# Performance work log

Measured on AMD Instinct MI355X. Metric: run time of the kernel, lower is better.

Reference implementation:

```python
import math
import jax, jax.numpy as jnp
import numpy as np

B, N, L, D, H = 1, 64, 512, 768, 12
DK = D // H


def setup_inputs() -> dict:
    rng = jax.random.key(0)
    ks = jax.random.split(rng, 8)
    s = 0.02  # weight init scale
    return {
        "query": jax.random.normal(ks[0], (B, N, L, D), jnp.float32),
        "key": jax.random.normal(ks[1], (B, N, L, D), jnp.float32),
        "value": jax.random.normal(ks[2], (B, N, L, D), jnp.float32),
        "Wq": jax.random.normal(ks[3], (D, D), jnp.float32) * s,
        "bq": jnp.zeros((D,), jnp.float32),
        "Wk": jax.random.normal(ks[4], (D, D), jnp.float32) * s,
        "bk": jnp.zeros((D,), jnp.float32),
        "Wv": jax.random.normal(ks[5], (D, D), jnp.float32) * s,
        "bv": jnp.zeros((D,), jnp.float32),
        "Wo": jax.random.normal(ks[6], (D, D), jnp.float32) * s,
        "bo": jnp.zeros((D,), jnp.float32),
    }


def reference(query, key, value, Wq, bq, Wk, bk, Wv, bv, Wo, bo):
    b, n, l, d = query.shape
    h, dk = H, DK
    # combined scaling: 1/sqrt(d_k) * 1/sqrt(N)
    scale = 1.0 / (math.sqrt(dk) * math.sqrt(n))
    # nn.Linear: y = x @ W.T + b  (W is [out, in])
    q = (jnp.einsum('bnld,ed->bnle', query, Wq) + bq).reshape(b, n, l, h, dk) * scale
    k = (jnp.einsum('bnld,ed->bnle', key, Wk) + bk).reshape(b, n, l, h, dk)
    v = (jnp.einsum('bnld,ed->bnle', value, Wv) + bv).reshape(b, n, l, h, dk)
    # tied attention: scores summed over the N (sequence-copy) axis BEFORE softmax
    att = jnp.einsum('bnihk,bnjhk->bhij', q, k)  # [B,H,L,L]
    att = jax.nn.softmax(att, axis=-1)  # dropout is identity in eval
    # single attention map broadcast across all N value tensors
    out = jnp.einsum('bhij,bnjhk->bnihk', att, v).reshape(b, n, l, d)
    return jnp.einsum('bnld,ed->bnle', out, Wo) + bo
```

## Files before the change

kernel.cpp:

```cpp
#include <hip/hip_runtime.h>


typedef __bf16 bf16x8 __attribute__((ext_vector_type(8)));
typedef float f32x4 __attribute__((ext_vector_type(4)));

__device__ __forceinline__ unsigned short f2bf(float f) {
  unsigned u = __float_as_uint(f);
  u += 0x7fffu + ((u >> 16) & 1u);
  return (unsigned short)(u >> 16);
}

__device__ __forceinline__ void gll16(const void* g, void* l) {
  __builtin_amdgcn_global_load_lds(
      (const __attribute__((address_space(1))) unsigned int*)g,
      (__attribute__((address_space(3))) unsigned int*)l, 16, 0, 0);
}

#define BAR __builtin_amdgcn_s_barrier()

enum { MODE_QCAT = 0, MODE_VT = 1, MODE_ATT = 2, MODE_OUTWS = 3, MODE_OUT_BIAS = 4 };

template <int MODE>
__global__ __launch_bounds__(512, 2) void gemm256(
    const void* __restrict__ Av, const void* __restrict__ Bv,
    const float* __restrict__ b0, const float* __restrict__ b1,
    void* __restrict__ Cv, int K, int lda, int ldb,
    long long a_bs, long long b_bs, float alpha0, float alpha1,
    long long c_bs, int ntn) {
  __shared__ unsigned short L[2][2][16384];

  const int tid = threadIdx.x;
  const int wave = tid >> 6;
  const int lane = tid & 63;
  const int wm = wave >> 2;
  const int wn = wave & 3;
  const int l15 = lane & 15;
  const int kq8 = lane >> 4;
  const int sw = l15 & 7;

  const int bid = blockIdx.x;
  const int xcd = bid & 7;
  const int kk_ = bid >> 3;
  const int tn = kk_ % ntn;
  const int tm = (kk_ / ntn) * 8 + xcd;
  const int batch = blockIdx.z;

  const long long m0 = (long long)tm * 256;
  const long long n0 = (long long)tn * 256;

  const unsigned short* Ab = (const unsigned short*)Av + (long long)batch * a_bs;
  const unsigned short* Bb = (const unsigned short*)Bv + (long long)batch * b_bs;

  const long long rowAw = m0 + wave * 8 + (lane >> 3);
  const long long rowBw = n0 + wave * 8 + (lane >> 3);
  const int csw = ((lane & 7) ^ (lane >> 3)) << 3;

  f32x4 acc[8][4] = {};

  auto stA = [&](int buf, int q, int k0) {
    gll16(Ab + (rowAw + (q << 6)) * (long long)lda + k0 + csw,
          &L[buf][0][(q << 12) + (wave << 9)]);
  };
  auto stB = [&](int buf, int q, int k0) {
    gll16(Bb + (rowBw + (q << 6)) * (long long)ldb + k0 + csw,
          &L[buf][1][(q << 12) + (wave << 9)]);
  };

  float bpre[4] = {};
  float aa = 1.0f;
  if constexpr (MODE == MODE_QCAT || MODE == MODE_VT || MODE == MODE_OUT_BIAS) {
    const float* bb = batch ? b1 : b0;
    aa = batch ? alpha1 : alpha0;
#pragma unroll
    for (int u = 0; u < 4; ++u) bpre[u] = bb[n0 + wn * 64 + u * 16 + l15];
  }

  const int NT = K >> 6;
#pragma unroll
  for (int q = 0; q < 4; ++q) stB(0, q, 0);
#pragma unroll
  for (int q = 0; q < 4; ++q) stA(0, q, 0);
  if (NT > 1) {
    stA(1, 0, 64);
    stA(1, 2, 64);
    asm volatile("s_waitcnt vmcnt(2)" ::: "memory");
  } else {
    asm volatile("s_waitcnt vmcnt(0)" ::: "memory");
  }
  BAR;

  for (int T = 0; T < NT; ++T) {
    const int cur = T & 1, nxt = cur ^ 1;
    const int k1 = (T + 1) << 6, k2 = (T + 2) << 6;
#pragma unroll
    for (int p = 0; p < 4; ++p) {
      const int kc = p >> 1, mh = p & 1;
      bf16x8 af[4], bfr[4];
#pragma unroll
      for (int mf = 0; mf < 4; ++mf) {
        const int row = wm * 128 + mh * 64 + mf * 16 + l15;
        af[mf] = *(const bf16x8*)&L[cur][0][row * 64 + (((kc << 2) + kq8) ^ sw) * 8];
      }
#pragma unroll
      for (int u = 0; u < 4; ++u) {
        const int row = wn * 64 + u * 16 + l15;
        bfr[u] = *(const bf16x8*)&L[cur][1][row * 64 + (((kc << 2) + kq8) ^ sw) * 8];
      }
      if (p == 0 && T + 1 < NT) { stB(nxt, 0, k1); stB(nxt, 1, k1); }
      if (p == 1 && T + 1 < NT) { stB(nxt, 2, k1); stB(nxt, 3, k1); }
      if (p == 2 && T + 1 < NT) { stA(nxt, 1, k1); stA(nxt, 3, k1); }
      if (p == 3 && T + 2 < NT) { stA(cur, 0, k2); stA(cur, 2, k2); }
      __builtin_amdgcn_s_setprio(1);
#pragma unroll
      for (int mf = 0; mf < 4; ++mf)
#pragma unroll
        for (int u = 0; u < 4; ++u)
          acc[mh * 4 + mf][u] = __builtin_amdgcn_mfma_f32_16x16x32_bf16(
              af[mf], bfr[u], acc[mh * 4 + mf][u], 0, 0, 0);
      __builtin_amdgcn_s_setprio(0);
      if (p == 3) {
        if (T + 1 < NT) {
          if (T + 2 < NT) asm volatile("s_waitcnt vmcnt(2)" ::: "memory");
          else            asm volatile("s_waitcnt vmcnt(0)" ::: "memory");
          BAR;
        }
      } else {
        BAR;
      }
    }
  }

#pragma unroll
  for (int mf = 0; mf < 8; ++mf) {
#pragma unroll
    for (int u = 0; u < 4; ++u) {
      const long long col = n0 + wn * 64 + u * 16 + l15;
#pragma unroll
      for (int r = 0; r < 4; ++r) {
        const long long row = m0 + wm * 128 + mf * 16 + (lane >> 4) * 4 + r;
        float v = acc[mf][u][r];
        if constexpr (MODE == MODE_QCAT) {
          const float vv = (v + bpre[u]) * aa;
          const long long h = col >> 6, kq = col & 63, n = row >> 9, i = row & 511;
          ((unsigned short*)Cv + batch * c_bs)[((h * 512 + i) << 12) + (n << 6) + kq] =
              f2bf(vv);
        } else if constexpr (MODE == MODE_VT) {
          const float vv = v + bpre[u];
          const long long h = col >> 6, kq = col & 63, n = row >> 9, j = row & 511;
          ((unsigned short*)Cv)[(((h << 12) + (n << 6) + kq) << 9) + j] = f2bf(vv);
        } else {
          ((float*)Cv)[row * 768 + col] = v + bpre[u];
        }
      }
    }
  }
}

constexpr int BM = 128, BN = 128, BK = 32;

template <int MODE, bool SWZ, int KS>
__global__ __launch_bounds__(256, 2) void gemm_bt(
    const void* __restrict__ Av, const void* __restrict__ Bv,
    const float* __restrict__ bias, void* __restrict__ Cv,
    int K, int lda, int ldb, long long a_bs, long long b_bs,
    float alpha, int ntn, long long c_bs) {
  constexpr int LP = 32;

  __shared__ unsigned short As0[BM * LP];
  __shared__ unsigned short Bs0[BN * LP];
  __shared__ unsigned short As1[BM * LP];
  __shared__ unsigned short Bs1[BN * LP];

  const int tid = threadIdx.x;
  const int wave = tid >> 6;
  const int lane = tid & 63;
  const int wm = wave >> 1, wn = wave & 1;

  int tm, tn, batch = 0, ks = 0;
  if constexpr (SWZ && MODE == MODE_ATT) {
    const int bid = blockIdx.x;
    const int xcd = bid & 7, j = bid >> 3;
    const int z = (j >> 4) * 8 + xcd;
    const int tile = j & 15;
    tn = tile & 3;
    tm = tile >> 2;
    ks = z % KS;
    batch = z / KS;
  } else if constexpr (SWZ && MODE == MODE_OUTWS) {
    const int bid = blockIdx.x;
    const int xcd = bid & 7, j = bid >> 3;
    const int g = (j >> 6) * 8 + xcd;
    const int idx = j & 63;
    batch = g >> 1;
    tm = idx >> 4;
    tn = (g & 1) * 16 + (idx & 15);
  } else {
    if constexpr (SWZ) {
      const int bid = blockIdx.x;
      const int xcd = bid & 7;
      const int k = bid >> 3;
      tn = k % ntn;
      tm = (k / ntn) * 8 + xcd;
    } else {
      tn = blockIdx.x;
      tm = blockIdx.y;
    }
    batch = blockIdx.z;
    if constexpr (KS > 1) { ks = batch % KS; batch /= KS; }
  }

  const long long m0 = (long long)tm * BM;
  const long long n0 = (long long)tn * BN;

  const unsigned short* Ab = (const unsigned short*)Av + (long long)batch * a_bs + (long long)ks * K;
  const unsigned short* Bb = (const unsigned short*)Bv + (long long)batch * b_bs + (long long)ks * K;

  f32x4 acc[4][4] = {};

  const int l15 = lane & 15;
  const int kq = (lane >> 4) * 8;
  const int r_in = lane >> 2;
  const int c8 = (lane & 3) * 8;

  auto stage = [&](unsigned short* Asb, unsigned short* Bsb, int k0) {
#pragma unroll
    for (int t = 0; t < 2; ++t) {
      const int rb = t * 64 + wave * 16;
      gll16(Ab + (m0 + rb + r_in) * (long long)lda + k0 + c8, &Asb[rb * LP]);
      gll16(Bb + (n0 + rb + r_in) * (long long)ldb + k0 + c8, &Bsb[rb * LP]);
    }
  };
  auto compute = [&](const unsigned short* Asb, const unsigned short* Bsb) {
    bf16x8 af[4], bfr[4];
#pragma unroll
    for (int t = 0; t < 4; ++t)
      af[t] = *(const bf16x8*)&Asb[(wm * 64 + t * 16 + l15) * LP + kq];
#pragma unroll
    for (int u = 0; u < 4; ++u)
      bfr[u] = *(const bf16x8*)&Bsb[(wn * 64 + u * 16 + l15) * LP + kq];
#pragma unroll
    for (int t = 0; t < 4; ++t)
#pragma unroll
      for (int u = 0; u < 4; ++u)
        acc[t][u] = __builtin_amdgcn_mfma_f32_16x16x32_bf16(af[t], bfr[u], acc[t][u], 0, 0, 0);
  };

  stage(As0, Bs0, 0);
  asm volatile("s_waitcnt vmcnt(0)" ::: "memory");
  BAR;

  const int NT = K >> 5;
  for (int t = 0; t < NT; t += 2) {
    stage(As1, Bs1, (t + 1) << 5);
    asm volatile("s_waitcnt vmcnt(4)" ::: "memory");
    BAR;
    compute(As0, Bs0);
    BAR;
    if (t + 2 < NT) {
      stage(As0, Bs0, (t + 2) << 5);
      asm volatile("s_waitcnt vmcnt(4)" ::: "memory");
    } else {
      asm volatile("s_waitcnt vmcnt(0)" ::: "memory");
    }
    BAR;
    compute(As1, Bs1);
    BAR;
  }

#pragma unroll
  for (int t = 0; t < 4; ++t) {
#pragma unroll
    for (int u = 0; u < 4; ++u) {
      const long long col = n0 + wn * 64 + u * 16 + l15;
#pragma unroll
      for (int r = 0; r < 4; ++r) {
        const long long row = m0 + wm * 64 + t * 16 + (lane >> 4) * 4 + r;
        float v = acc[t][u][r];
        if constexpr (MODE == MODE_ATT) {
          float* p = &((float*)Cv)[((long long)batch << 18) + (row << 9) + col];
          if constexpr (KS > 1) atomicAdd(p, v); else *p = v;
        } else if constexpr (MODE == MODE_OUTWS) {
          const long long n = col >> 6, kk = col & 63;
          ((unsigned short*)Cv)[(n * 512 + row) * 768 + (long long)batch * 64 + kk] = f2bf(v);
        } else {
          ((float*)Cv)[row * 768 + col] = v + alpha;
        }
      }
    }
  }
}

__global__ __launch_bounds__(256) void softmax_rows(const float* __restrict__ att,
                                                    unsigned short* __restrict__ outb) {
  const long long rowbase = (long long)blockIdx.x << 9;
  const int tid = threadIdx.x;
  float a = att[rowbase + tid];
  float b = att[rowbase + tid + 256];

  float m = fmaxf(a, b);
#pragma unroll
  for (int off = 32; off; off >>= 1) m = fmaxf(m, __shfl_down(m, off));
  __shared__ float redm[4];
  if ((tid & 63) == 0) redm[tid >> 6] = m;
  __syncthreads();
  m = fmaxf(fmaxf(redm[0], redm[1]), fmaxf(redm[2], redm[3]));

  const float e0 = __expf(a - m), e1 = __expf(b - m);
  float s = e0 + e1;
#pragma unroll
  for (int off = 32; off; off >>= 1) s += __shfl_down(s, off);
  __shared__ float reds[4];
  if ((tid & 63) == 0) reds[tid >> 6] = s;
  __syncthreads();
  s = reds[0] + reds[1] + reds[2] + reds[3];

  const float inv = 1.0f / s;
  outb[rowbase + tid] = f2bf(e0 * inv);
  outb[rowbase + tid + 256] = f2bf(e1 * inv);
}

__global__ __launch_bounds__(256) void cvt_bf16(const float* __restrict__ in,
                                                unsigned short* __restrict__ out) {
  const long long i = ((long long)blockIdx.x * 256 + threadIdx.x) * 8;
  const float4 a = *(const float4*)(in + i);
  const float4 b = *(const float4*)(in + i + 4);
  uint4 p;
  p.x = (unsigned)f2bf(a.x) | ((unsigned)f2bf(a.y) << 16);
  p.y = (unsigned)f2bf(a.z) | ((unsigned)f2bf(a.w) << 16);
  p.z = (unsigned)f2bf(b.x) | ((unsigned)f2bf(b.y) << 16);
  p.w = (unsigned)f2bf(b.z) | ((unsigned)f2bf(b.w) << 16);
  *(uint4*)(out + i) = p;
}

__global__ __launch_bounds__(256) void cvt_qk(
    const float* __restrict__ s0, const float* __restrict__ s1,
    unsigned short* __restrict__ d0, unsigned short* __restrict__ d1) {
  const float* s = blockIdx.y ? s1 : s0;
  unsigned short* d = blockIdx.y ? d1 : d0;
  const long long i = ((long long)blockIdx.x * 256 + threadIdx.x) * 8;
  const float4 a = *(const float4*)(s + i);
  const float4 b = *(const float4*)(s + i + 4);
  uint4 p;
  p.x = (unsigned)f2bf(a.x) | ((unsigned)f2bf(a.y) << 16);
  p.y = (unsigned)f2bf(a.z) | ((unsigned)f2bf(a.w) << 16);
  p.z = (unsigned)f2bf(b.x) | ((unsigned)f2bf(b.y) << 16);
  p.w = (unsigned)f2bf(b.z) | ((unsigned)f2bf(b.w) << 16);
  *(uint4*)(d + i) = p;
}

__global__ __launch_bounds__(256) void cvt_w4(
    const float* __restrict__ s0, const float* __restrict__ s1,
    const float* __restrict__ s2, const float* __restrict__ s3,
    unsigned short* __restrict__ d0, unsigned short* __restrict__ d1,
    unsigned short* __restrict__ d2, unsigned short* __restrict__ d3) {
  const float* s;
  unsigned short* d;
  switch (blockIdx.y) {
    case 0: s = s0; d = d0; break;
    case 1: s = s1; d = d1; break;
    case 2: s = s2; d = d2; break;
    default: s = s3; d = d3; break;
  }
  const long long i = ((long long)blockIdx.x * 256 + threadIdx.x) * 8;
  const float4 a = *(const float4*)(s + i);
  const float4 b = *(const float4*)(s + i + 4);
  uint4 p;
  p.x = (unsigned)f2bf(a.x) | ((unsigned)f2bf(a.y) << 16);
  p.y = (unsigned)f2bf(a.z) | ((unsigned)f2bf(a.w) << 16);
  p.z = (unsigned)f2bf(b.x) | ((unsigned)f2bf(b.y) << 16);
  p.w = (unsigned)f2bf(b.z) | ((unsigned)f2bf(b.w) << 16);
  *(uint4*)(d + i) = p;
}

extern "C" void kernel_launch(void* const* d_in, const int* in_sizes, int n_in,
                              void* d_out, int out_size, void* d_ws, size_t ws_size,
                              hipStream_t stream) {
  const float* query = (const float*)d_in[0];
  const float* key   = (const float*)d_in[1];
  const float* value = (const float*)d_in[2];
  const float* Wq = (const float*)d_in[3];
  const float* bq = (const float*)d_in[4];
  const float* Wk = (const float*)d_in[5];
  const float* bk = (const float*)d_in[6];
  const float* Wv = (const float*)d_in[7];
  const float* bv = (const float*)d_in[8];
  const float* Wo = (const float*)d_in[9];
  const float* bo = (const float*)d_in[10];
  float* out = (float*)d_out;

  char* ws = (char*)d_ws;
  unsigned short* q_ws  = (unsigned short*)(ws);
  unsigned short* k_ws  = (unsigned short*)(ws + 50331648);
  unsigned short* vt_ws = (unsigned short*)(ws + 100663296);
  float*          att   = (float*)(ws + 150994944);
  unsigned short* wo_b  = (unsigned short*)(ws + 163577856);
  unsigned short* wq_b  = (unsigned short*)(ws + 150994944);
  unsigned short* wk_b  = (unsigned short*)(ws + 150994944 + 1179648);
  unsigned short* wv_b  = (unsigned short*)(ws + 150994944 + 2359296);
  unsigned short* att_b = k_ws;
  unsigned short* out_ws = q_ws;
  unsigned short* xb0 = (unsigned short*)d_out;
  unsigned short* xb1 = (unsigned short*)d_out + 25165824;
  (void)wk_b; (void)wv_b;

  const dim3 blk(256);
  const dim3 blk5(512);

  cvt_w4<<<dim3(288, 4), blk, 0, stream>>>(Wo, Wq, Wk, Wv, wo_b, wq_b, wk_b, wv_b);

  cvt_qk<<<dim3(12288, 2), blk, 0, stream>>>(query, key, xb0, xb1);

  gemm256<MODE_QCAT><<<dim3(384, 1, 2), blk5, 0, stream>>>(
      xb0, wq_b, bq, bk, q_ws, 768, 768, 768, 25165824LL, 589824LL,
      0.015625f, 1.0f, 25165824LL, 3);

  cvt_bf16<<<12288, blk, 0, stream>>>(value, xb0);
  gemm256<MODE_VT><<<dim3(384, 1, 1), blk5, 0, stream>>>(
      xb0, wv_b, bv, nullptr, vt_ws, 768, 768, 768, 0, 0, 1.0f, 1.0f, 0, 3);

  hipMemsetAsync(att, 0, 12582912, stream);
  gemm_bt<MODE_ATT, true, 4><<<dim3(768, 1, 1), blk, 0, stream>>>(
      q_ws, k_ws, nullptr, att, 1024, 4096, 4096, 2097152LL, 2097152LL, 1.0f, 0, 0);

  softmax_rows<<<6144, blk, 0, stream>>>(att, att_b);

  gemm_bt<MODE_OUTWS, true, 1><<<dim3(1536, 1, 1), blk, 0, stream>>>(
      att_b, vt_ws, nullptr, out_ws, 512, 512, 512, 262144LL, 2097152LL, 1.0f, 0, 0);

  gemm256<MODE_OUT_BIAS><<<dim3(384, 1, 1), blk5, 0, stream>>>(
      out_ws, wo_b, bo, nullptr, out, 768, 768, 768, 0, 0, 1.0f, 1.0f, 0, 3);
}
```

Baseline: 633.3 us.

## Simplify gemm256 pipeline and replace split-K atomics with partial buffers

Rewrites the 256x256 GEMM main loop to use two 32-wide K halves with a simpler stage/compute/wait-all-barrier pattern, halving LDS use and dropping the XOR swizzle. The attention split-K GEMM now writes four separate partial score buffers instead of atomically adding into a zeroed buffer, so the memset and atomics go away and softmax sums the partials on load. The trade-off is more memory traffic in softmax, possible LDS bank conflicts without the swizzle, and a coarser vmcnt(0) wait that reduces load/compute overlap.

```diff
diff --git a/kernel.cpp b/kernel.cpp
--- a/kernel.cpp
+++ b/kernel.cpp
@@ -17,6 +17,7 @@
 }
 
 #define BAR __builtin_amdgcn_s_barrier()
+#define VM0_BAR asm volatile("s_waitcnt vmcnt(0)\ns_barrier" ::: "memory")
 
 enum { MODE_QCAT = 0, MODE_VT = 1, MODE_ATT = 2, MODE_OUTWS = 3, MODE_OUT_BIAS = 4 };
 
@@ -27,7 +28,7 @@
     void* __restrict__ Cv, int K, int lda, int ldb,
     long long a_bs, long long b_bs, float alpha0, float alpha1,
     long long c_bs, int ntn) {
-  __shared__ unsigned short L[2][2][16384];
+  __shared__ unsigned short L[2][2][8192];
 
   const int tid = threadIdx.x;
   const int wave = tid >> 6;
@@ -36,13 +37,12 @@
   const int wn = wave & 3;
   const int l15 = lane & 15;
   const int kq8 = lane >> 4;
-  const int sw = l15 & 7;
 
   const int bid = blockIdx.x;
   const int xcd = bid & 7;
-  const int kk_ = bid >> 3;
-  const int tn = kk_ % ntn;
-  const int tm = (kk_ / ntn) * 8 + xcd;
+  const int j = bid >> 3;
+  const int tn = j % ntn;
+  const int tm = (j / ntn) * 8 + xcd;
   const int batch = blockIdx.z;
 
   const long long m0 = (long long)tm * 256;
@@ -51,19 +51,47 @@
   const unsigned short* Ab = (const unsigned short*)Av + (long long)batch * a_bs;
   const unsigned short* Bb = (const unsigned short*)Bv + (long long)batch * b_bs;
 
-  const long long rowAw = m0 + wave * 8 + (lane >> 3);
-  const long long rowBw = n0 + wave * 8 + (lane >> 3);
-  const int csw = ((lane & 7) ^ (lane >> 3)) << 3;
-
   f32x4 acc[8][4] = {};
 
-  auto stA = [&](int buf, int q, int k0) {
-    gll16(Ab + (rowAw + (q << 6)) * (long long)lda + k0 + csw,
-          &L[buf][0][(q << 12) + (wave << 9)]);
+  const int srow = lane >> 2;
+  const int scol = (lane & 3) * 8;
+
+  auto stageA = [&](int h, int kT) {
+#pragma unroll
+    for (int r = 0; r < 2; ++r) {
+      const int c = wave + r * 8;
+      gll16(Ab + (m0 + c * 16 + srow) * (long long)lda + kT + h * 32 + scol,
+            &L[0][h][c * 512]);
+    }
   };
-  auto stB = [&](int buf, int q, int k0) {
-    gll16(Bb + (rowBw + (q << 6)) * (long long)ldb + k0 + csw,
-          &L[buf][1][(q << 12) + (wave << 9)]);
+  auto stageB = [&](int h, int kT) {
+#pragma unroll
+    for (int r = 0; r < 2; ++r) {
+      const int c = wave + r * 8;
+      gll16(Bb + (n0 + c * 16 + srow) * (long long)ldb + kT + h * 32 + scol,
+            &L[1][h][c * 512]);
+    }
+  };
+
+  auto compute = [&](int h) {
+    bf16x8 af[8], bfr[4];
+#pragma unroll
+    for (int q = 0; q < 8; ++q) {
+      const int row = wm * 128 + q * 16 + l15;
+      af[q] = *(const bf16x8*)&L[0][h][row * 32 + kq8 * 8];
+    }
+#pragma unroll
+    for (int u = 0; u < 4; ++u) {
+      const int row = wn * 64 + u * 16 + l15;
+      bfr[u] = *(const bf16x8*)&L[1][h][row * 32 + kq8 * 8];
+    }
+    __builtin_amdgcn_s_setprio(1);
+#pragma unroll
+    for (int q = 0; q < 8; ++q)
+#pragma unroll
+      for (int u = 0; u < 4; ++u)
+        acc[q][u] = __builtin_amdgcn_mfma_f32_16x16x32_bf16(af[q], bfr[u], acc[q][u], 0, 0, 0);
+    __builtin_amdgcn_s_setprio(0);
   };
 
   float bpre[4] = {};
@@ -76,78 +104,45 @@
   }
 
   const int NT = K >> 6;
-#pragma unroll
-  for (int q = 0; q < 4; ++q) stB(0, q, 0);
-#pragma unroll
-  for (int q = 0; q < 4; ++q) stA(0, q, 0);
-  if (NT > 1) {
-    stA(1, 0, 64);
-    stA(1, 2, 64);
-    asm volatile("s_waitcnt vmcnt(2)" ::: "memory");
-  } else {
-    asm volatile("s_waitcnt vmcnt(0)" ::: "memory");
-  }
-  BAR;
+
+  stageA(0, 0);
+  stageB(0, 0);
+  VM0_BAR;
 
   for (int T = 0; T < NT; ++T) {
-    const int cur = T & 1, nxt = cur ^ 1;
-    const int k1 = (T + 1) << 6, k2 = (T + 2) << 6;
-#pragma unroll
-    for (int p = 0; p < 4; ++p) {
-      const int kc = p >> 1, mh = p & 1;
-      bf16x8 af[4], bfr[4];
-#pragma unroll
-      for (int mf = 0; mf < 4; ++mf) {
-        const int row = wm * 128 + mh * 64 + mf * 16 + l15;
-        af[mf] = *(const bf16x8*)&L[cur][0][row * 64 + (((kc << 2) + kq8) ^ sw) * 8];
-      }
-#pragma unroll
-      for (int u = 0; u < 4; ++u) {
-        const int row = wn * 64 + u * 16 + l15;
-        bfr[u] = *(const bf16x8*)&L[cur][1][row * 64 + (((kc << 2) + kq8) ^ sw) * 8];
-      }
-      if (p == 0 && T + 1 < NT) { stB(nxt, 0, k1); stB(nxt, 1, k1); }
-      if (p == 1 && T + 1 < NT) { stB(nxt, 2, k1); stB(nxt, 3, k1); }
-      if (p == 2 && T + 1 < NT) { stA(nxt, 1, k1); stA(nxt, 3, k1); }
-      if (p == 3 && T + 2 < NT) { stA(cur, 0, k2); stA(cur, 2, k2); }
-      __builtin_amdgcn_s_setprio(1);
-#pragma unroll
-      for (int mf = 0; mf < 4; ++mf)
-#pragma unroll
-        for (int u = 0; u < 4; ++u)
-          acc[mh * 4 + mf][u] = __builtin_amdgcn_mfma_f32_16x16x32_bf16(
-              af[mf], bfr[u], acc[mh * 4 + mf][u], 0, 0, 0);
-      __builtin_amdgcn_s_setprio(0);
-      if (p == 3) {
-        if (T + 1 < NT) {
-          if (T + 2 < NT) asm volatile("s_waitcnt vmcnt(2)" ::: "memory");
-          else            asm volatile("s_waitcnt vmcnt(0)" ::: "memory");
-          BAR;
-        }
-      } else {
-        BAR;
-      }
-    }
-  }
-
-#pragma unroll
-  for (int mf = 0; mf < 8; ++mf) {
+    const int kT = T << 6;
+    stageA(1, kT);
+    stageB(1, kT);
+    compute(0);
+    VM0_BAR;
+    if (T + 1 < NT) {
+      stageA(0, kT + 64);
+      stageB(0, kT + 64);
+      compute(1);
+      VM0_BAR;
+    } else {
+      compute(1);
+    }
+  }
+
+#pragma unroll
+  for (int q = 0; q < 8; ++q) {
 #pragma unroll
     for (int u = 0; u < 4; ++u) {
       const long long col = n0 + wn * 64 + u * 16 + l15;
 #pragma unroll
       for (int r = 0; r < 4; ++r) {
-        const long long row = m0 + wm * 128 + mf * 16 + (lane >> 4) * 4 + r;
-        float v = acc[mf][u][r];
+        const long long row = m0 + wm * 128 + q * 16 + (lane >> 4) * 4 + r;
+        float v = acc[q][u][r];
         if constexpr (MODE == MODE_QCAT) {
           const float vv = (v + bpre[u]) * aa;
-          const long long h = col >> 6, kq = col & 63, n = row >> 9, i = row & 511;
-          ((unsigned short*)Cv + batch * c_bs)[((h * 512 + i) << 12) + (n << 6) + kq] =
+          const long long h = col >> 6, kk = col & 63, n = row >> 9, i = row & 511;
+          ((unsigned short*)Cv + batch * c_bs)[((h * 512 + i) << 12) + (n << 6) + kk] =
               f2bf(vv);
         } else if constexpr (MODE == MODE_VT) {
           const float vv = v + bpre[u];
-          const long long h = col >> 6, kq = col & 63, n = row >> 9, j = row & 511;
-          ((unsigned short*)Cv)[(((h << 12) + (n << 6) + kq) << 9) + j] = f2bf(vv);
+          const long long h = col >> 6, kk = col & 63, n = row >> 9, jj = row & 511;
+          ((unsigned short*)Cv)[(((h << 12) + (n << 6) + kk) << 9) + jj] = f2bf(vv);
         } else {
           ((float*)Cv)[row * 768 + col] = v + bpre[u];
         }
@@ -195,16 +190,8 @@
     tm = idx >> 4;
     tn = (g & 1) * 16 + (idx & 15);
   } else {
-    if constexpr (SWZ) {
-      const int bid = blockIdx.x;
-      const int xcd = bid & 7;
-      const int k = bid >> 3;
-      tn = k % ntn;
-      tm = (k / ntn) * 8 + xcd;
-    } else {
-      tn = blockIdx.x;
-      tm = blockIdx.y;
-    }
+    tn = blockIdx.x;
+    tm = blockIdx.y;
     batch = blockIdx.z;
     if constexpr (KS > 1) { ks = batch % KS; batch /= KS; }
   }
@@ -277,8 +264,7 @@
         const long long row = m0 + wm * 64 + t * 16 + (lane >> 4) * 4 + r;
         float v = acc[t][u][r];
         if constexpr (MODE == MODE_ATT) {
-          float* p = &((float*)Cv)[((long long)batch << 18) + (row << 9) + col];
-          if constexpr (KS > 1) atomicAdd(p, v); else *p = v;
+          ((float*)Cv)[((long long)(ks * 12 + batch) << 18) + (row << 9) + col] = v;
         } else if constexpr (MODE == MODE_OUTWS) {
           const long long n = col >> 6, kk = col & 63;
           ((unsigned short*)Cv)[(n * 512 + row) * 768 + (long long)batch * 64 + kk] = f2bf(v);
@@ -294,8 +280,12 @@
                                                     unsigned short* __restrict__ outb) {
   const long long rowbase = (long long)blockIdx.x << 9;
   const int tid = threadIdx.x;
-  float a = att[rowbase + tid];
-  float b = att[rowbase + tid + 256];
+  float a = 0.0f, b = 0.0f;
+#pragma unroll
+  for (int s = 0; s < 4; ++s) {
+    a += att[(long long)s * 3145728 + rowbase + tid];
+    b += att[(long long)s * 3145728 + rowbase + tid + 256];
+  }
 
   float m = fmaxf(a, b);
 #pragma unroll
@@ -392,21 +382,20 @@
   unsigned short* q_ws  = (unsigned short*)(ws);
   unsigned short* k_ws  = (unsigned short*)(ws + 50331648);
   unsigned short* vt_ws = (unsigned short*)(ws + 100663296);
-  float*          att   = (float*)(ws + 150994944);
-  unsigned short* wo_b  = (unsigned short*)(ws + 163577856);
   unsigned short* wq_b  = (unsigned short*)(ws + 150994944);
   unsigned short* wk_b  = (unsigned short*)(ws + 150994944 + 1179648);
   unsigned short* wv_b  = (unsigned short*)(ws + 150994944 + 2359296);
+  unsigned short* wo_b  = (unsigned short*)(ws + 150994944 + 3538944);
   unsigned short* att_b = k_ws;
   unsigned short* out_ws = q_ws;
   unsigned short* xb0 = (unsigned short*)d_out;
   unsigned short* xb1 = (unsigned short*)d_out + 25165824;
-  (void)wk_b; (void)wv_b;
+  float* att_part = (float*)((char*)d_out + 50331648);
 
   const dim3 blk(256);
   const dim3 blk5(512);
 
-  cvt_w4<<<dim3(288, 4), blk, 0, stream>>>(Wo, Wq, Wk, Wv, wo_b, wq_b, wk_b, wv_b);
+  cvt_w4<<<dim3(288, 4), blk, 0, stream>>>(Wq, Wk, Wv, Wo, wq_b, wk_b, wv_b, wo_b);
 
   cvt_qk<<<dim3(12288, 2), blk, 0, stream>>>(query, key, xb0, xb1);
 
@@ -418,14 +407,15 @@
   gemm256<MODE_VT><<<dim3(384, 1, 1), blk5, 0, stream>>>(
       xb0, wv_b, bv, nullptr, vt_ws, 768, 768, 768, 0, 0, 1.0f, 1.0f, 0, 3);
 
-  hipMemsetAsync(att, 0, 12582912, stream);
   gemm_bt<MODE_ATT, true, 4><<<dim3(768, 1, 1), blk, 0, stream>>>(
-      q_ws, k_ws, nullptr, att, 1024, 4096, 4096, 2097152LL, 2097152LL, 1.0f, 0, 0);
-
-  softmax_rows<<<6144, blk, 0, stream>>>(att, att_b);
+      q_ws, k_ws, nullptr, att_part, 1024, 4096, 4096, 2097152LL, 2097152LL,
+      1.0f, 0, 0);
+
+  softmax_rows<<<6144, blk, 0, stream>>>(att_part, att_b);
 
   gemm_bt<MODE_OUTWS, true, 1><<<dim3(1536, 1, 1), blk, 0, stream>>>(
-      att_b, vt_ws, nullptr, out_ws, 512, 512, 512, 262144LL, 2097152LL, 1.0f, 0, 0);
+      att_b, vt_ws, nullptr, out_ws, 512, 512, 512, 262144LL, 2097152LL,
+      1.0f, 0, 0);
 
   gemm256<MODE_OUT_BIAS><<<dim3(384, 1, 1), blk5, 0, stream>>>(
       out_ws, wo_b, bo, nullptr, out, 768, 768, 768, 0, 0, 1.0f, 1.0f, 0, 3);
```

Result: slower. 1.260 ms (+98.9%).
